# Kernel optimization log

Hardware: AMD Instinct MI355X
Metric: run time of the kernel (lower is better)

The kernel has to match this reference:

```python
import jax, jax.numpy as jnp
import numpy as np

N_NODES = 50000


def _gcn_norm(edge_index, n_nodes):
    # Add self-loops, then symmetric normalization D^-1/2 (A+I) D^-1/2 (GCNConv default).
    src = jnp.concatenate([edge_index[0], jnp.arange(n_nodes)])
    dst = jnp.concatenate([edge_index[1], jnp.arange(n_nodes)])
    deg = jax.ops.segment_sum(jnp.ones_like(src, dtype=jnp.float32), dst, num_segments=n_nodes)
    dinv = jnp.where(deg > 0, jax.lax.rsqrt(jnp.maximum(deg, 1.0)), 0.0)
    norm = dinv[src] * dinv[dst]  # [E + N]
    return src, dst, norm


def _gcn_conv(x, W, b, src, dst, norm, n_nodes):
    h = x @ W                      # [N, F_out] transform first (fewer bytes moved)
    msg = h[src] * norm[:, None]   # gather per-edge
    out = jax.ops.segment_sum(msg, dst, num_segments=n_nodes)  # scatter-add
    return out + b


def setup_inputs() -> dict:
    key = jax.random.key(0)
    k_x, k_e, k1, k2, k3, k4, k5, k6 = jax.random.split(key, 8)
    in_dim, hid, out_dim, n_edges = 128, 128, 64, 800000
    s = lambda fan_in: 1.0 / np.sqrt(fan_in)
    return {
        "x": jax.random.normal(k_x, (N_NODES, in_dim), dtype=jnp.float32),
        "edge_index": jax.random.randint(k_e, (2, n_edges), 0, N_NODES),
        "W1": jax.random.uniform(k1, (in_dim, hid), jnp.float32, -s(in_dim), s(in_dim)),
        "b1": jnp.zeros((hid,), jnp.float32),
        "W_mu": jax.random.uniform(k2, (hid, out_dim), jnp.float32, -s(hid), s(hid)),
        "b_mu": jnp.zeros((out_dim,), jnp.float32),
        "W_logstd": jax.random.uniform(k3, (hid, out_dim), jnp.float32, -s(hid), s(hid)),
        "b_logstd": jnp.zeros((out_dim,), jnp.float32),
    }


def reference(x, edge_index, W1, b1, W_mu, b_mu, W_logstd, b_logstd):
    src, dst, norm = _gcn_norm(edge_index, N_NODES)
    h = jax.nn.relu(_gcn_conv(x, W1, b1, src, dst, norm, N_NODES))
    mu = _gcn_conv(h, W_mu, b_mu, src, dst, norm, N_NODES)
    logstd = _gcn_conv(h, W_logstd, b_logstd, src, dst, norm, N_NODES)
    return mu, logstd
```

## Files before the change

### kernel.cpp

```cpp
#include <hip/hip_runtime.h>
#include <hip/hip_bf16.h>

#define N_NODES 50000
#define FDIM 128
#define NPAD 50176
#define SCAN_NB 49

typedef short bf16x8 __attribute__((ext_vector_type(8)));
typedef float f32x4  __attribute__((ext_vector_type(4)));

__device__ __forceinline__ unsigned short rne_bf16(float f) {
    unsigned int u = __float_as_uint(f);
    unsigned int r = (u + 0x7FFFu + ((u >> 16) & 1u)) >> 16;
    return (unsigned short)r;
}
__device__ __forceinline__ float bf16_to_f32(unsigned short s) {
    return __uint_as_float(((unsigned int)s) << 16);
}
__device__ __forceinline__ void split_bf16(float f, unsigned short& h, unsigned short& l) {
    h = rne_bf16(f);
    l = rne_bf16(f - bf16_to_f32(h));
}
__device__ __forceinline__ void unpack2(unsigned int d, float& f0, float& f1) {
    f0 = __uint_as_float(d << 16);
    f1 = __uint_as_float(d & 0xFFFF0000u);
}
__device__ __forceinline__ void acc_row(const uint4& m, float wt, float* a) {
    float f0, f1;
    unpack2(m.x, f0, f1); a[0] += wt * f0; a[1] += wt * f1;
    unpack2(m.y, f0, f1); a[2] += wt * f0; a[3] += wt * f1;
    unpack2(m.z, f0, f1); a[4] += wt * f0; a[5] += wt * f1;
    unpack2(m.w, f0, f1); a[6] += wt * f0; a[7] += wt * f1;
}

__global__ __launch_bounds__(256) void zero_kernel(int4* __restrict__ p, int n4) {
    int i = blockIdx.x * 256 + threadIdx.x;
    if (i < n4) p[i] = make_int4(0, 0, 0, 0);
}

__global__ __launch_bounds__(256) void count_kernel(const int* __restrict__ dst,
                                                    int* __restrict__ counts,
                                                    int* __restrict__ rank, int E) {
    int e = blockIdx.x * blockDim.x + threadIdx.x;
    if (e < E) rank[e] = atomicAdd(&counts[dst[e]], 1);
}

__global__ __launch_bounds__(256) void scan_local_kernel(const int* __restrict__ counts,
                                                         int* __restrict__ local,
                                                         int* __restrict__ bsums,
                                                         float* __restrict__ dinv) {
    int t    = threadIdx.x;
    int lane = t & 63;
    int wid  = t >> 6;
    int base = blockIdx.x * 1024 + t * 4;
    int4 v = *(const int4*)(counts + base);
    float4 dv;
    dv.x = rsqrtf((float)v.x + 1.0f);
    dv.y = rsqrtf((float)v.y + 1.0f);
    dv.z = rsqrtf((float)v.z + 1.0f);
    dv.w = rsqrtf((float)v.w + 1.0f);
    *(float4*)(dinv + base) = dv;
    int s = v.x + v.y + v.z + v.w;
    int incl = s;
#pragma unroll
    for (int off = 1; off < 64; off <<= 1) {
        int u = __shfl_up(incl, off, 64);
        if (lane >= off) incl += u;
    }
    __shared__ int wtot[4];
    if (lane == 63) wtot[wid] = incl;
    __syncthreads();
    int wbase = 0;
#pragma unroll
    for (int w = 0; w < 3; w++) wbase += (w < wid) ? wtot[w] : 0;
    int excl = wbase + incl - s;
    int4 o;
    o.x = excl;
    o.y = excl + v.x;
    o.z = o.y + v.y;
    o.w = o.z + v.z;
    *(int4*)(local + base) = o;
    if (t == 255) bsums[blockIdx.x] = wbase + incl;
}

__global__ __launch_bounds__(64) void scan_bsums_kernel(const int* __restrict__ bsums,
                                                        int* __restrict__ boffs, int nb) {
    int lane = threadIdx.x;
    int v = (lane < nb) ? bsums[lane] : 0;
    int incl = v;
#pragma unroll
    for (int off = 1; off < 64; off <<= 1) {
        int u = __shfl_up(incl, off, 64);
        if (lane >= off) incl += u;
    }
    if (lane < nb) boffs[lane] = incl - v;
}

__global__ __launch_bounds__(256) void scan_add_kernel(const int* __restrict__ local,
                                                       const int* __restrict__ boffs,
                                                       int* __restrict__ offsets) {
    int base = blockIdx.x * 1024 + threadIdx.x * 4;
    int bo = boffs[blockIdx.x];
    int4 v = *(const int4*)(local + base);
    v.x += bo; v.y += bo; v.z += bo; v.w += bo;
    *(int4*)(offsets + base) = v;
}

__global__ __launch_bounds__(256) void scatter_kernel(const int* __restrict__ src,
                                                      const int* __restrict__ dst,
                                                      const int* __restrict__ rank,
                                                      const int* __restrict__ offsets,
                                                      int* __restrict__ csr_src, int E) {
    int e = blockIdx.x * blockDim.x + threadIdx.x;
    if (e < E) {
        int d = dst[e];
        int pos = offsets[d] + rank[e];
        csr_src[pos] = src[e];
    }
}

__global__ __launch_bounds__(256) void cvt_x_kernel(const float* __restrict__ x,
                                                    unsigned short* __restrict__ xb, int n4) {
    int i = blockIdx.x * blockDim.x + threadIdx.x;
    if (i >= n4) return;
    float4 v = ((const float4*)x)[i];
    unsigned int d0 = (unsigned int)rne_bf16(v.x) | ((unsigned int)rne_bf16(v.y) << 16);
    unsigned int d1 = (unsigned int)rne_bf16(v.z) | ((unsigned int)rne_bf16(v.w) << 16);
    ((uint2*)xb)[i] = make_uint2(d0, d1);
}

__global__ __launch_bounds__(256) void cvt_w_kernel(const float* __restrict__ W1,
                                                    const float* __restrict__ Wmu,
                                                    const float* __restrict__ Wlog,
                                                    unsigned short* __restrict__ W1thi,
                                                    unsigned short* __restrict__ W1tlo,
                                                    unsigned short* __restrict__ Wcthi,
                                                    unsigned short* __restrict__ Wctlo) {
    int tid = blockIdx.x * 256 + threadIdx.x;
    int n = tid & 127, k = tid >> 7;
    int swzidx = (n * 128 + k) ^ ((n & 7) << 3);
    unsigned short h, l;
    float v1 = W1[k * 128 + n];
    split_bf16(v1, h, l);
    W1thi[swzidx] = h;
    W1tlo[swzidx] = l;
    float v2 = (n < 64) ? Wmu[k * 64 + n] : Wlog[k * 64 + (n - 64)];
    split_bf16(v2, h, l);
    Wcthi[swzidx] = h;
    Wctlo[swzidx] = l;
}

__global__ __launch_bounds__(256) void agg_bf16_kernel(const unsigned short* __restrict__ X,
                                                       const int* __restrict__ offsets,
                                                       const int* __restrict__ csr_src,
                                                       const float* __restrict__ dinv,
                                                       unsigned short* __restrict__ Yhi,
                                                       unsigned short* __restrict__ Ylo,
                                                       int n) {
    int node = (blockIdx.x << 4) + (threadIdx.x >> 4);
    int l16  = threadIdx.x & 15;
    if (node >= n) return;
    const uint4* X16 = (const uint4*)X;

    float dv = dinv[node];
    float sw = dv * dv;
    float a[8];
    {
        uint4 xv = X16[(size_t)node * 16 + l16];
        float f0, f1;
        unpack2(xv.x, f0, f1); a[0] = sw * f0; a[1] = sw * f1;
        unpack2(xv.y, f0, f1); a[2] = sw * f0; a[3] = sw * f1;
        unpack2(xv.z, f0, f1); a[4] = sw * f0; a[5] = sw * f1;
        unpack2(xv.w, f0, f1); a[6] = sw * f0; a[7] = sw * f1;
    }

    int beg = offsets[node], end = offsets[node + 1];
    int i = beg;
    for (; i + 4 <= end; i += 4) {
        int s0 = csr_src[i];
        int s1 = csr_src[i + 1];
        int s2 = csr_src[i + 2];
        int s3 = csr_src[i + 3];
        uint4 m0 = X16[(size_t)s0 * 16 + l16];
        uint4 m1 = X16[(size_t)s1 * 16 + l16];
        uint4 m2 = X16[(size_t)s2 * 16 + l16];
        uint4 m3 = X16[(size_t)s3 * 16 + l16];
        float w0 = dv * dinv[s0];
        float w1 = dv * dinv[s1];
        float w2 = dv * dinv[s2];
        float w3 = dv * dinv[s3];
        acc_row(m0, w0, a);
        acc_row(m1, w1, a);
        acc_row(m2, w2, a);
        acc_row(m3, w3, a);
    }
    for (; i < end; i++) {
        int s = csr_src[i];
        uint4 m = X16[(size_t)s * 16 + l16];
        acc_row(m, dv * dinv[s], a);
    }

    unsigned short h[8], l[8];
#pragma unroll
    for (int j = 0; j < 8; j++) split_bf16(a[j], h[j], l[j]);
    uint4 ph, pl;
    ph.x = (unsigned int)h[0] | ((unsigned int)h[1] << 16);
    ph.y = (unsigned int)h[2] | ((unsigned int)h[3] << 16);
    ph.z = (unsigned int)h[4] | ((unsigned int)h[5] << 16);
    ph.w = (unsigned int)h[6] | ((unsigned int)h[7] << 16);
    pl.x = (unsigned int)l[0] | ((unsigned int)l[1] << 16);
    pl.y = (unsigned int)l[2] | ((unsigned int)l[3] << 16);
    pl.z = (unsigned int)l[4] | ((unsigned int)l[5] << 16);
    pl.w = (unsigned int)l[6] | ((unsigned int)l[7] << 16);
    ((uint4*)Yhi)[(size_t)node * 16 + l16] = ph;
    ((uint4*)Ylo)[(size_t)node * 16 + l16] = pl;
}

template <int EPI>
__global__ __launch_bounds__(256) void mfma_gemm_kernel(const unsigned short* __restrict__ Ahi,
                                                        const unsigned short* __restrict__ Alo,
                                                        const unsigned short* __restrict__ Wthi,
                                                        const unsigned short* __restrict__ Wtlo,
                                                        const float* __restrict__ ba,
                                                        const float* __restrict__ bb,
                                                        unsigned short* __restrict__ H,
                                                        float* __restrict__ out, int M) {
    __shared__ unsigned short Wlds[32768];

    int t    = threadIdx.x;
    int wave = t >> 6;
    int lane = t & 63;
    int m16  = lane & 15;
    int kg   = lane >> 4;

    {
        const uint4* gh = (const uint4*)Wthi;
        const uint4* gl = (const uint4*)Wtlo;
        uint4* lds4 = (uint4*)Wlds;
#pragma unroll
        for (int i = 0; i < 8; i++) lds4[i * 256 + t] = gh[i * 256 + t];
#pragma unroll
        for (int i = 0; i < 8; i++) lds4[2048 + i * 256 + t] = gl[i * 256 + t];
    }

    int rbase = blockIdx.x * 64 + wave * 16;
    int arow  = rbase + m16;
    bool rok  = arow < M;
    const unsigned short* arh = Ahi + (size_t)(rok ? arow : 0) * 128;
    const unsigned short* arl = Alo + (size_t)(rok ? arow : 0) * 128;
    bf16x8 ah[4], al[4];
#pragma unroll
    for (int kt = 0; kt < 4; kt++) {
        bf16x8 vh = *(const bf16x8*)(const void*)(arh + kt * 32 + kg * 8);
        bf16x8 vl = *(const bf16x8*)(const void*)(arl + kt * 32 + kg * 8);
        ah[kt] = rok ? vh : (bf16x8)(short)0;
        al[kt] = rok ? vl : (bf16x8)(short)0;
    }
    __syncthreads();

    int swz = (m16 & 7) << 3;
#pragma unroll
    for (int np = 0; np < 4; np++) {
        int nt0 = np * 2, nt1 = np * 2 + 1;
        f32x4 acc0 = {0.f, 0.f, 0.f, 0.f};
        f32x4 acc1 = {0.f, 0.f, 0.f, 0.f};
#pragma unroll
        for (int kt = 0; kt < 4; kt++) {
            int i0 = (((nt0 * 16 + m16) * 128) + kt * 32 + kg * 8) ^ swz;
            int i1 = (((nt1 * 16 + m16) * 128) + kt * 32 + kg * 8) ^ swz;
            bf16x8 bh0 = *(const bf16x8*)(const void*)&Wlds[i0];
            bf16x8 bl0 = *(const bf16x8*)(const void*)&Wlds[16384 + i0];
            bf16x8 bh1 = *(const bf16x8*)(const void*)&Wlds[i1];
            bf16x8 bl1 = *(const bf16x8*)(const void*)&Wlds[16384 + i1];
            acc0 = __builtin_amdgcn_mfma_f32_16x16x32_bf16(ah[kt], bh0, acc0, 0, 0, 0);
            acc1 = __builtin_amdgcn_mfma_f32_16x16x32_bf16(ah[kt], bh1, acc1, 0, 0, 0);
            acc0 = __builtin_amdgcn_mfma_f32_16x16x32_bf16(ah[kt], bl0, acc0, 0, 0, 0);
            acc1 = __builtin_amdgcn_mfma_f32_16x16x32_bf16(ah[kt], bl1, acc1, 0, 0, 0);
            acc0 = __builtin_amdgcn_mfma_f32_16x16x32_bf16(al[kt], bh0, acc0, 0, 0, 0);
            acc1 = __builtin_amdgcn_mfma_f32_16x16x32_bf16(al[kt], bh1, acc1, 0, 0, 0);
        }
#pragma unroll
        for (int half = 0; half < 2; half++) {
            int nt = half ? nt1 : nt0;
            const f32x4& acc = half ? acc1 : acc0;
            int n0 = nt * 16 + m16;
            if (EPI == 0) {
                float b = ba[n0];
#pragma unroll
                for (int j = 0; j < 4; j++) {
                    int r = rbase + kg * 4 + j;
                    if (r < M) H[(size_t)r * 128 + n0] = rne_bf16(fmaxf(acc[j] + b, 0.f));
                }
            } else {
                bool is_mu = (n0 < 64);
                int c = is_mu ? n0 : (n0 - 64);
                float b = is_mu ? ba[c] : bb[c];
                size_t obase = is_mu ? 0 : (size_t)N_NODES * 64;
#pragma unroll
                for (int j = 0; j < 4; j++) {
                    int r = rbase + kg * 4 + j;
                    if (r < M) out[obase + (size_t)r * 64 + c] = acc[j] + b;
                }
            }
        }
    }
}

extern "C" void kernel_launch(void* const* d_in, const int* in_sizes, int n_in,
                              void* d_out, int out_size, void* d_ws, size_t ws_size,
                              hipStream_t stream) {
    const float* x    = (const float*)d_in[0];
    const int*   ei   = (const int*)d_in[1];
    const float* W1   = (const float*)d_in[2];
    const float* b1   = (const float*)d_in[3];
    const float* Wmu  = (const float*)d_in[4];
    const float* bmu  = (const float*)d_in[5];
    const float* Wlog = (const float*)d_in[6];
    const float* blog = (const float*)d_in[7];
    float* out = (float*)d_out;

    const int N = N_NODES;
    const int E = in_sizes[1] / 2;
    const int* src = ei;
    const int* dst = ei + E;

    auto align256 = [](size_t v) { return (v + 255) & ~(size_t)255; };
    char* ws = (char*)d_ws;
    size_t off = 0;
    int*   counts  = (int*)(ws + off);  off += align256((size_t)NPAD * 4);
    int*   offsets = (int*)(ws + off);  off += align256((size_t)NPAD * 4);
    int*   local   = (int*)(ws + off);  off += align256((size_t)NPAD * 4);
    int*   bsums   = (int*)(ws + off);  off += align256(256 * 4);
    int*   boffs   = (int*)(ws + off);  off += align256(256 * 4);
    float* dinv    = (float*)(ws + off); off += align256((size_t)NPAD * 4);
    int*   rank    = (int*)(ws + off);  off += align256((size_t)E * 4);
    int*   csr_src = (int*)(ws + off);  off += align256((size_t)E * 4);
    unsigned short* xb    = (unsigned short*)(ws + off); off += align256((size_t)N * FDIM * 2);
    unsigned short* Hb    = (unsigned short*)(ws + off); off += align256((size_t)N * FDIM * 2);
    unsigned short* Aghi  = (unsigned short*)(ws + off); off += align256((size_t)N * FDIM * 2);
    unsigned short* Aglo  = (unsigned short*)(ws + off); off += align256((size_t)N * FDIM * 2);
    unsigned short* W1thi = (unsigned short*)(ws + off); off += align256(128 * 128 * 2);
    unsigned short* W1tlo = (unsigned short*)(ws + off); off += align256(128 * 128 * 2);
    unsigned short* Wcthi = (unsigned short*)(ws + off); off += align256(128 * 128 * 2);
    unsigned short* Wctlo = (unsigned short*)(ws + off); off += align256(128 * 128 * 2);

    zero_kernel<<<(NPAD / 4 + 255) / 256, 256, 0, stream>>>((int4*)counts, NPAD / 4);
    count_kernel<<<(E + 255) / 256, 256, 0, stream>>>(dst, counts, rank, E);
    scan_local_kernel<<<SCAN_NB, 256, 0, stream>>>(counts, local, bsums, dinv);
    scan_bsums_kernel<<<1, 64, 0, stream>>>(bsums, boffs, SCAN_NB);
    scan_add_kernel<<<SCAN_NB, 256, 0, stream>>>(local, boffs, offsets);
    scatter_kernel<<<(E + 255) / 256, 256, 0, stream>>>(src, dst, rank, offsets, csr_src, E);

    cvt_x_kernel<<<(N * FDIM / 4 + 255) / 256, 256, 0, stream>>>(x, xb, N * FDIM / 4);
    cvt_w_kernel<<<64, 256, 0, stream>>>(W1, Wmu, Wlog, W1thi, W1tlo, Wcthi, Wctlo);

    agg_bf16_kernel<<<(N + 15) / 16, 256, 0, stream>>>(xb, offsets, csr_src, dinv, Aghi, Aglo, N);

    mfma_gemm_kernel<0><<<(N + 63) / 64, 256, 0, stream>>>(Aghi, Aglo, W1thi, W1tlo,
                                                           b1, nullptr, Hb, nullptr, N);

    agg_bf16_kernel<<<(N + 15) / 16, 256, 0, stream>>>(Hb, offsets, csr_src, dinv, Aghi, Aglo, N);

    mfma_gemm_kernel<1><<<(N + 63) / 64, 256, 0, stream>>>(Aghi, Aglo, Wcthi, Wctlo,
                                                           bmu, blog, nullptr, out, N);
}
```

Measured before the change: 176.3 us.

## Pre-scale features by dinv, pad CSR rows to multiples of four, enlarge GEMM blocks

Source features are pre-multiplied by D^-1/2 (in the x conversion and in the first GEMM epilogue), so the aggregation loop becomes a plain sum. That drops the per-edge dinv gather and multiply, and the destination scale is applied once at the end. CSR rows are padded to multiples of four with a dummy zero row, which allows vectorized int4 index loads and an unrolled-by-8 gather with no scalar tail. The block-sum scan kernel is folded into scan_add, and GEMM blocks grow to 512 threads covering 128 rows. The costs are extra padded edges, a larger csr buffer, and scaling in bf16 before rounding, which changes numerics slightly.

```diff
diff --git a/kernel.cpp b/kernel.cpp
--- a/kernel.cpp
+++ b/kernel.cpp
@@ -25,12 +25,12 @@
     f0 = __uint_as_float(d << 16);
     f1 = __uint_as_float(d & 0xFFFF0000u);
 }
-__device__ __forceinline__ void acc_row(const uint4& m, float wt, float* a) {
+__device__ __forceinline__ void add_row(const uint4& m, float* a) {
     float f0, f1;
-    unpack2(m.x, f0, f1); a[0] += wt * f0; a[1] += wt * f1;
-    unpack2(m.y, f0, f1); a[2] += wt * f0; a[3] += wt * f1;
-    unpack2(m.z, f0, f1); a[4] += wt * f0; a[5] += wt * f1;
-    unpack2(m.w, f0, f1); a[6] += wt * f0; a[7] += wt * f1;
+    unpack2(m.x, f0, f1); a[0] += f0; a[1] += f1;
+    unpack2(m.y, f0, f1); a[2] += f0; a[3] += f1;
+    unpack2(m.z, f0, f1); a[4] += f0; a[5] += f1;
+    unpack2(m.w, f0, f1); a[6] += f0; a[7] += f1;
 }
 
 __global__ __launch_bounds__(256) void zero_kernel(int4* __restrict__ p, int n4) {
@@ -53,13 +53,18 @@
     int lane = t & 63;
     int wid  = t >> 6;
     int base = blockIdx.x * 1024 + t * 4;
-    int4 v = *(const int4*)(counts + base);
+    int4 c = *(const int4*)(counts + base);
     float4 dv;
-    dv.x = rsqrtf((float)v.x + 1.0f);
-    dv.y = rsqrtf((float)v.y + 1.0f);
-    dv.z = rsqrtf((float)v.z + 1.0f);
-    dv.w = rsqrtf((float)v.w + 1.0f);
+    dv.x = (base + 0 < N_NODES) ? rsqrtf((float)c.x + 1.0f) : 0.f;
+    dv.y = (base + 1 < N_NODES) ? rsqrtf((float)c.y + 1.0f) : 0.f;
+    dv.z = (base + 2 < N_NODES) ? rsqrtf((float)c.z + 1.0f) : 0.f;
+    dv.w = (base + 3 < N_NODES) ? rsqrtf((float)c.w + 1.0f) : 0.f;
     *(float4*)(dinv + base) = dv;
+    int4 v;
+    v.x = (c.x + 3) & ~3;
+    v.y = (c.y + 3) & ~3;
+    v.z = (c.z + 3) & ~3;
+    v.w = (c.w + 3) & ~3;
     int s = v.x + v.y + v.z + v.w;
     int incl = s;
 #pragma unroll
@@ -83,27 +88,41 @@
     if (t == 255) bsums[blockIdx.x] = wbase + incl;
 }
 
-__global__ __launch_bounds__(64) void scan_bsums_kernel(const int* __restrict__ bsums,
-                                                        int* __restrict__ boffs, int nb) {
-    int lane = threadIdx.x;
-    int v = (lane < nb) ? bsums[lane] : 0;
-    int incl = v;
-#pragma unroll
-    for (int off = 1; off < 64; off <<= 1) {
-        int u = __shfl_up(incl, off, 64);
-        if (lane >= off) incl += u;
-    }
-    if (lane < nb) boffs[lane] = incl - v;
-}
-
 __global__ __launch_bounds__(256) void scan_add_kernel(const int* __restrict__ local,
-                                                       const int* __restrict__ boffs,
-                                                       int* __restrict__ offsets) {
-    int base = blockIdx.x * 1024 + threadIdx.x * 4;
-    int bo = boffs[blockIdx.x];
+                                                       const int* __restrict__ bsums,
+                                                       const int* __restrict__ counts,
+                                                       int* __restrict__ offsets,
+                                                       int* __restrict__ csr_src,
+                                                       unsigned short* __restrict__ xb,
+                                                       unsigned short* __restrict__ Hb) {
+    int t = threadIdx.x;
+    __shared__ int s_bo;
+    if (t < 64) {
+        int v = (t < blockIdx.x) ? bsums[t] : 0;
+#pragma unroll
+        for (int off = 32; off; off >>= 1) v += __shfl_down(v, off, 64);
+        if (t == 0) s_bo = v;
+    }
+    if (blockIdx.x == 0 && t >= 64 && t < 128) {
+        int k = t - 64;
+        ((unsigned int*)(xb + (size_t)N_NODES * 128))[k] = 0u;
+        ((unsigned int*)(Hb + (size_t)N_NODES * 128))[k] = 0u;
+    }
+    __syncthreads();
+    int bo = s_bo;
+    int base = blockIdx.x * 1024 + t * 4;
     int4 v = *(const int4*)(local + base);
+    int4 c = *(const int4*)(counts + base);
     v.x += bo; v.y += bo; v.z += bo; v.w += bo;
     *(int4*)(offsets + base) = v;
+    int off0[4] = {v.x, v.y, v.z, v.w};
+    int cr[4]   = {c.x, c.y, c.z, c.w};
+#pragma unroll
+    for (int k = 0; k < 4; k++) {
+        int b = off0[k] + cr[k];
+        int e = off0[k] + ((cr[k] + 3) & ~3);
+        for (int j = b; j < e; j++) csr_src[j] = N_NODES;
+    }
 }
 
 __global__ __launch_bounds__(256) void scatter_kernel(const int* __restrict__ src,
@@ -120,10 +139,13 @@
 }
 
 __global__ __launch_bounds__(256) void cvt_x_kernel(const float* __restrict__ x,
+                                                    const float* __restrict__ dinv,
                                                     unsigned short* __restrict__ xb, int n4) {
     int i = blockIdx.x * blockDim.x + threadIdx.x;
     if (i >= n4) return;
+    float dv = dinv[i >> 5];
     float4 v = ((const float4*)x)[i];
+    v.x *= dv; v.y *= dv; v.z *= dv; v.w *= dv;
     unsigned int d0 = (unsigned int)rne_bf16(v.x) | ((unsigned int)rne_bf16(v.y) << 16);
     unsigned int d1 = (unsigned int)rne_bf16(v.z) | ((unsigned int)rne_bf16(v.w) << 16);
     ((uint2*)xb)[i] = make_uint2(d0, d1);
@@ -162,47 +184,45 @@
     if (node >= n) return;
     const uint4* X16 = (const uint4*)X;
 
-    float dv = dinv[node];
-    float sw = dv * dv;
     float a[8];
     {
         uint4 xv = X16[(size_t)node * 16 + l16];
         float f0, f1;
-        unpack2(xv.x, f0, f1); a[0] = sw * f0; a[1] = sw * f1;
-        unpack2(xv.y, f0, f1); a[2] = sw * f0; a[3] = sw * f1;
-        unpack2(xv.z, f0, f1); a[4] = sw * f0; a[5] = sw * f1;
-        unpack2(xv.w, f0, f1); a[6] = sw * f0; a[7] = sw * f1;
+        unpack2(xv.x, f0, f1); a[0] = f0; a[1] = f1;
+        unpack2(xv.y, f0, f1); a[2] = f0; a[3] = f1;
+        unpack2(xv.z, f0, f1); a[4] = f0; a[5] = f1;
+        unpack2(xv.w, f0, f1); a[6] = f0; a[7] = f1;
     }
 
     int beg = offsets[node], end = offsets[node + 1];
     int i = beg;
-    for (; i + 4 <= end; i += 4) {
-        int s0 = csr_src[i];
-        int s1 = csr_src[i + 1];
-        int s2 = csr_src[i + 2];
-        int s3 = csr_src[i + 3];
-        uint4 m0 = X16[(size_t)s0 * 16 + l16];
-        uint4 m1 = X16[(size_t)s1 * 16 + l16];
-        uint4 m2 = X16[(size_t)s2 * 16 + l16];
-        uint4 m3 = X16[(size_t)s3 * 16 + l16];
-        float w0 = dv * dinv[s0];
-        float w1 = dv * dinv[s1];
-        float w2 = dv * dinv[s2];
-        float w3 = dv * dinv[s3];
-        acc_row(m0, w0, a);
-        acc_row(m1, w1, a);
-        acc_row(m2, w2, a);
-        acc_row(m3, w3, a);
-    }
-    for (; i < end; i++) {
-        int s = csr_src[i];
-        uint4 m = X16[(size_t)s * 16 + l16];
-        acc_row(m, dv * dinv[s], a);
-    }
-
+    for (; i + 8 <= end; i += 8) {
+        int4 q0 = *(const int4*)(csr_src + i);
+        int4 q1 = *(const int4*)(csr_src + i + 4);
+        uint4 m0 = X16[(size_t)q0.x * 16 + l16];
+        uint4 m1 = X16[(size_t)q0.y * 16 + l16];
+        uint4 m2 = X16[(size_t)q0.z * 16 + l16];
+        uint4 m3 = X16[(size_t)q0.w * 16 + l16];
+        uint4 m4 = X16[(size_t)q1.x * 16 + l16];
+        uint4 m5 = X16[(size_t)q1.y * 16 + l16];
+        uint4 m6 = X16[(size_t)q1.z * 16 + l16];
+        uint4 m7 = X16[(size_t)q1.w * 16 + l16];
+        add_row(m0, a); add_row(m1, a); add_row(m2, a); add_row(m3, a);
+        add_row(m4, a); add_row(m5, a); add_row(m6, a); add_row(m7, a);
+    }
+    if (i < end) {
+        int4 q0 = *(const int4*)(csr_src + i);
+        uint4 m0 = X16[(size_t)q0.x * 16 + l16];
+        uint4 m1 = X16[(size_t)q0.y * 16 + l16];
+        uint4 m2 = X16[(size_t)q0.z * 16 + l16];
+        uint4 m3 = X16[(size_t)q0.w * 16 + l16];
+        add_row(m0, a); add_row(m1, a); add_row(m2, a); add_row(m3, a);
+    }
+
+    float dv = dinv[node];
     unsigned short h[8], l[8];
 #pragma unroll
-    for (int j = 0; j < 8; j++) split_bf16(a[j], h[j], l[j]);
+    for (int j = 0; j < 8; j++) split_bf16(a[j] * dv, h[j], l[j]);
     uint4 ph, pl;
     ph.x = (unsigned int)h[0] | ((unsigned int)h[1] << 16);
     ph.y = (unsigned int)h[2] | ((unsigned int)h[3] << 16);
@@ -217,12 +237,13 @@
 }
 
 template <int EPI>
-__global__ __launch_bounds__(256) void mfma_gemm_kernel(const unsigned short* __restrict__ Ahi,
+__global__ __launch_bounds__(512) void mfma_gemm_kernel(const unsigned short* __restrict__ Ahi,
                                                         const unsigned short* __restrict__ Alo,
                                                         const unsigned short* __restrict__ Wthi,
                                                         const unsigned short* __restrict__ Wtlo,
                                                         const float* __restrict__ ba,
                                                         const float* __restrict__ bb,
+                                                        const float* __restrict__ dinv,
                                                         unsigned short* __restrict__ H,
                                                         float* __restrict__ out, int M) {
     __shared__ unsigned short Wlds[32768];
@@ -238,12 +259,12 @@
         const uint4* gl = (const uint4*)Wtlo;
         uint4* lds4 = (uint4*)Wlds;
 #pragma unroll
-        for (int i = 0; i < 8; i++) lds4[i * 256 + t] = gh[i * 256 + t];
-#pragma unroll
-        for (int i = 0; i < 8; i++) lds4[2048 + i * 256 + t] = gl[i * 256 + t];
-    }
-
-    int rbase = blockIdx.x * 64 + wave * 16;
+        for (int i = 0; i < 4; i++) lds4[i * 512 + t] = gh[i * 512 + t];
+#pragma unroll
+        for (int i = 0; i < 4; i++) lds4[2048 + i * 512 + t] = gl[i * 512 + t];
+    }
+
+    int rbase = blockIdx.x * 128 + wave * 16;
     int arow  = rbase + m16;
     bool rok  = arow < M;
     const unsigned short* arh = Ahi + (size_t)(rok ? arow : 0) * 128;
@@ -256,6 +277,8 @@
         ah[kt] = rok ? vh : (bf16x8)(short)0;
         al[kt] = rok ? vl : (bf16x8)(short)0;
     }
+    float4 dv4 = {1.f, 1.f, 1.f, 1.f};
+    if (EPI == 0) dv4 = *(const float4*)(dinv + rbase + kg * 4);
     __syncthreads();
 
     int swz = (m16 & 7) << 3;
@@ -289,7 +312,10 @@
 #pragma unroll
                 for (int j = 0; j < 4; j++) {
                     int r = rbase + kg * 4 + j;
-                    if (r < M) H[(size_t)r * 128 + n0] = rne_bf16(fmaxf(acc[j] + b, 0.f));
+                    if (r < M) {
+                        float v = fmaxf(acc[j] + b, 0.f) * dv4[j];
+                        H[(size_t)r * 128 + n0] = rne_bf16(v);
+                    }
                 }
             } else {
                 bool is_mu = (n0 < 64);
@@ -321,6 +347,7 @@
 
     const int N = N_NODES;
     const int E = in_sizes[1] / 2;
+    const int Emax = E + 3 * N;
     const int* src = ei;
     const int* dst = ei + E;
 
@@ -331,12 +358,11 @@
     int*   offsets = (int*)(ws + off);  off += align256((size_t)NPAD * 4);
     int*   local   = (int*)(ws + off);  off += align256((size_t)NPAD * 4);
     int*   bsums   = (int*)(ws + off);  off += align256(256 * 4);
-    int*   boffs   = (int*)(ws + off);  off += align256(256 * 4);
     float* dinv    = (float*)(ws + off); off += align256((size_t)NPAD * 4);
     int*   rank    = (int*)(ws + off);  off += align256((size_t)E * 4);
-    int*   csr_src = (int*)(ws + off);  off += align256((size_t)E * 4);
-    unsigned short* xb    = (unsigned short*)(ws + off); off += align256((size_t)N * FDIM * 2);
-    unsigned short* Hb    = (unsigned short*)(ws + off); off += align256((size_t)N * FDIM * 2);
+    int*   csr_src = (int*)(ws + off);  off += align256((size_t)Emax * 4);
+    unsigned short* xb    = (unsigned short*)(ws + off); off += align256((size_t)(N + 1) * FDIM * 2);
+    unsigned short* Hb    = (unsigned short*)(ws + off); off += align256((size_t)(N + 1) * FDIM * 2);
     unsigned short* Aghi  = (unsigned short*)(ws + off); off += align256((size_t)N * FDIM * 2);
     unsigned short* Aglo  = (unsigned short*)(ws + off); off += align256((size_t)N * FDIM * 2);
     unsigned short* W1thi = (unsigned short*)(ws + off); off += align256(128 * 128 * 2);
@@ -347,20 +373,20 @@
     zero_kernel<<<(NPAD / 4 + 255) / 256, 256, 0, stream>>>((int4*)counts, NPAD / 4);
     count_kernel<<<(E + 255) / 256, 256, 0, stream>>>(dst, counts, rank, E);
     scan_local_kernel<<<SCAN_NB, 256, 0, stream>>>(counts, local, bsums, dinv);
-    scan_bsums_kernel<<<1, 64, 0, stream>>>(bsums, boffs, SCAN_NB);
-    scan_add_kernel<<<SCAN_NB, 256, 0, stream>>>(local, boffs, offsets);
+    scan_add_kernel<<<SCAN_NB, 256, 0, stream>>>(local, bsums, counts, offsets,
+                                                 csr_src, xb, Hb);
     scatter_kernel<<<(E + 255) / 256, 256, 0, stream>>>(src, dst, rank, offsets, csr_src, E);
 
-    cvt_x_kernel<<<(N * FDIM / 4 + 255) / 256, 256, 0, stream>>>(x, xb, N * FDIM / 4);
+    cvt_x_kernel<<<(N * FDIM / 4 + 255) / 256, 256, 0, stream>>>(x, dinv, xb, N * FDIM / 4);
     cvt_w_kernel<<<64, 256, 0, stream>>>(W1, Wmu, Wlog, W1thi, W1tlo, Wcthi, Wctlo);
 
     agg_bf16_kernel<<<(N + 15) / 16, 256, 0, stream>>>(xb, offsets, csr_src, dinv, Aghi, Aglo, N);
 
-    mfma_gemm_kernel<0><<<(N + 63) / 64, 256, 0, stream>>>(Aghi, Aglo, W1thi, W1tlo,
-                                                           b1, nullptr, Hb, nullptr, N);
+    mfma_gemm_kernel<0><<<(N + 127) / 128, 512, 0, stream>>>(Aghi, Aglo, W1thi, W1tlo,
+                                                             b1, nullptr, dinv, Hb, nullptr, N);
 
     agg_bf16_kernel<<<(N + 15) / 16, 256, 0, stream>>>(Hb, offsets, csr_src, dinv, Aghi, Aglo, N);
 
-    mfma_gemm_kernel<1><<<(N + 63) / 64, 256, 0, stream>>>(Aghi, Aglo, Wcthi, Wctlo,
-                                                           bmu, blog, nullptr, out, N);
-}
+    mfma_gemm_kernel<1><<<(N + 127) / 128, 512, 0, stream>>>(Aghi, Aglo, Wcthi, Wctlo,
+                                                             bmu, blog, nullptr, nullptr, out, N);
+}
```

Result: faster. 163.6 us (-7.2%).
